# Kernel optimization log

Hardware: AMD Instinct MI355X
Metric: run time of the kernel (lower is better)

Reference implementation:

```python
import jax, jax.numpy as jnp
import numpy as np

T, B, N_LABELS = 128, 512, 512
HIDDEN, SEMANTIC = 1024, 1024
THRESHOLD, DECAY = 1.0, 0.95


def setup_inputs() -> dict:
    key = jax.random.key(0)
    k1, k2, k3 = jax.random.split(key, 3)
    spike_seq = (jax.random.uniform(k1, (T, B, N_LABELS)) < 0.1).astype(jnp.float32)
    W1 = jax.random.normal(k2, (HIDDEN, N_LABELS), dtype=jnp.float32) * 0.05
    W2 = jax.random.normal(k3, (SEMANTIC, HIDDEN), dtype=jnp.float32) * 0.05
    return {"spike_seq": spike_seq, "W1": W1, "W2": W2}


def reference(spike_seq, W1, W2):
    """LIF two-layer SNN. LIF step: v = decay*v + input; spike = (v > threshold);
    hard reset to zero on spike. Returns time-averaged spikes of layer1 and layer2."""
    dtype = spike_seq.dtype
    Bsz = spike_seq.shape[1]

    def lif(v, x):
        v = DECAY * v + x
        spk = (v > THRESHOLD).astype(dtype)
        return spk, v * (1.0 - spk)

    def step(carry, x_t):
        v1, v2 = carry
        spk1, v1 = lif(v1, x_t @ W1.T)          # (B, HIDDEN)
        spk2, v2 = lif(v2, spk1 @ W2.T)         # (B, SEMANTIC)
        return (v1, v2), (spk1, spk2)

    v1_0 = jnp.zeros((Bsz, W1.shape[0]), dtype)
    v2_0 = jnp.zeros((Bsz, W2.shape[0]), dtype)
    _, (spk1_all, spk2_all) = jax.lax.scan(step, (v1_0, v2_0), spike_seq)
    return spk1_all.mean(axis=0), spk2_all.mean(axis=0)
```

## Files before the change

kernel.cpp:

```cpp
#include <hip/hip_runtime.h>


#define T_STEPS 128
#define BATCH   512
#define NLAB    512
#define HID     1024
#define SEM     1024
#define KCW     5

__global__ __launch_bounds__(256) void transpose32(const float* __restrict__ in,
                                                   float* __restrict__ out,
                                                   int R, int C) {
    __shared__ float tile[32][33];
    const int c0 = blockIdx.x * 32, r0 = blockIdx.y * 32;
    const int x = threadIdx.x, y0 = threadIdx.y;
#pragma unroll
    for (int i = 0; i < 32; i += 8)
        tile[y0 + i][x] = in[(size_t)(r0 + y0 + i) * C + (c0 + x)];
    __syncthreads();
#pragma unroll
    for (int i = 0; i < 32; i += 8)
        out[(size_t)(c0 + y0 + i) * R + (r0 + x)] = tile[x][y0 + i];
}

__device__ __forceinline__ float gather_chain(const int* __restrict__ list,
                                              int lo, int hi,
                                              const float* __restrict__ base,
                                              int tid, float s) {
    int k = lo;
    for (; k + 8 <= hi; k += 8) {
        float w[8];
#pragma unroll
        for (int j = 0; j < 8; ++j) {
            const int row = __builtin_amdgcn_readfirstlane(list[k + j]);
            w[j] = base[((size_t)row << 10) + tid];
        }
#pragma unroll
        for (int j = 0; j < 8; ++j)
            s = __fadd_rn(s, w[j]);
    }
    for (; k < hi; ++k) {
        const int row = __builtin_amdgcn_readfirstlane(list[k]);
        s = __fadd_rn(s, base[((size_t)row << 10) + tid]);
    }
    return s;
}

__global__ __launch_bounds__(1024, 8)
void snn_kernel(const float* __restrict__ spikes,
                const float* __restrict__ w1t,
                const float* __restrict__ w2t,
                float* __restrict__ out) {
    __shared__ int wc1[8];
    __shared__ int wc2[16];
    __shared__ __align__(16) int list1[NLAB];
    __shared__ __align__(16) int list2[HID];

    const int b    = blockIdx.x;
    const int tid  = threadIdx.x;
    const int w    = tid >> 6;
    const int lane = tid & 63;

    float v1 = 0.0f, v2 = 0.0f;
    int c1 = 0, c2 = 0;
    const float* sp_b = spikes + (size_t)b * NLAB;

    for (int t = 0; t < T_STEPS; ++t) {
        bool act = false;
        int pre1 = 0;
        if (tid < NLAB) {
            act = (sp_b[(size_t)t * (BATCH * NLAB) + tid] != 0.0f);
            const unsigned long long m = __ballot(act);
            pre1 = __popcll(m & ((1ull << lane) - 1ull));
            if (lane == 0) wc1[w] = __popcll(m);
        }
        __syncthreads();

        if (act) {
            int base = 0;
            for (int i = 0; i < w; ++i) base += wc1[i];
            list1[base + pre1] = tid;
        }
        __syncthreads();

        bool spk;
        int pre2 = 0;
        {
            int nA = 0, n1 = 0;
            {
                int s = 0;
#pragma unroll
                for (int i = 0; i < 8; ++i) { s += wc1[i]; if (i == KCW - 1) nA = s; }
                n1 = s;
            }
            const float x1 = __fadd_rn(gather_chain(list1, 0,  nA, w1t, tid, 0.0f),
                                       gather_chain(list1, nA, n1, w1t, tid, 0.0f));

            v1 = __fadd_rn(__fmul_rn(0.95f, v1), x1);
            spk = (v1 > 1.0f);
            if (spk) { c1++; v1 = 0.0f; }

            const unsigned long long m = __ballot(spk);
            pre2 = __popcll(m & ((1ull << lane) - 1ull));
            if (lane == 0) wc2[w] = __popcll(m);
        }
        __syncthreads();

        if (spk) {
            int base = 0;
            for (int i = 0; i < w; ++i) base += wc2[i];
            list2[base + pre2] = tid;
        }
        __syncthreads();

        {
            int nA = 0, nB = 0, nC = 0, n2 = 0;
            {
                int s = 0;
#pragma unroll
                for (int i = 0; i < 16; ++i) {
                    s += wc2[i];
                    if (i == KCW - 1)     nA = s;
                    if (i == 2 * KCW - 1) nB = s;
                    if (i == 3 * KCW - 1) nC = s;
                }
                n2 = s;
            }
            const float t1 = gather_chain(list2, 0,  nA, w2t, tid, 0.0f);
            const float t2 = gather_chain(list2, nA, nB, w2t, tid, 0.0f);
            const float t3 = gather_chain(list2, nB, nC, w2t, tid, 0.0f);
            const float t4 = gather_chain(list2, nC, n2, w2t, tid, 0.0f);
            const float x2 = __fadd_rn(__fadd_rn(__fadd_rn(t1, t2), t3), t4);

            v2 = __fadd_rn(__fmul_rn(0.95f, v2), x2);
            if (v2 > 1.0f) { c2++; v2 = 0.0f; }
        }
        __syncthreads();
    }

    out[(size_t)b * HID + tid]                       = (float)c1 * (1.0f / 128.0f);
    out[(size_t)BATCH * HID + (size_t)b * SEM + tid] = (float)c2 * (1.0f / 128.0f);
}

extern "C" void kernel_launch(void* const* d_in, const int* in_sizes, int n_in,
                              void* d_out, int out_size, void* d_ws, size_t ws_size,
                              hipStream_t stream) {
    const float* spikes = (const float*)d_in[0];
    const float* W1     = (const float*)d_in[1];
    const float* W2     = (const float*)d_in[2];
    float* out = (float*)d_out;

    float* w1t = (float*)d_ws;
    float* w2t = w1t + (size_t)NLAB * HID;

    dim3 tb(32, 8);
    transpose32<<<dim3(NLAB / 32, HID / 32), tb, 0, stream>>>(W1, w1t, HID, NLAB);
    transpose32<<<dim3(HID / 32, SEM / 32),  tb, 0, stream>>>(W2, w2t, SEM, HID);

    snn_kernel<<<BATCH, 1024, 0, stream>>>(spikes, w1t, w2t, out);
}
```

Baseline: 1.767 ms.

## Use 256-thread blocks with four neurons per thread and float4 weight gathers

Shrinks each block from 1024 to 256 threads, with every thread now owning four consecutive hidden or semantic neurons. Weight rows are gathered as float4 and spike inputs are read as float2. The compaction lists, ballots and chain split points are rebuilt so the summation order matches the earlier split. The aim is fewer, wider memory transactions and cheaper barriers across fewer waves, at the cost of more registers per thread and less latency hiding from wave count.

```diff
diff --git a/kernel.cpp b/kernel.cpp
--- a/kernel.cpp
+++ b/kernel.cpp
@@ -6,7 +6,6 @@
 #define NLAB    512
 #define HID     1024
 #define SEM     1024
-#define KCW     5
 
 __global__ __launch_bounds__(256) void transpose32(const float* __restrict__ in,
                                                    float* __restrict__ out,
@@ -23,36 +22,47 @@
         out[(size_t)(c0 + y0 + i) * R + (r0 + x)] = tile[x][y0 + i];
 }
 
-__device__ __forceinline__ float gather_chain(const int* __restrict__ list,
-                                              int lo, int hi,
-                                              const float* __restrict__ base,
-                                              int tid, float s) {
+__device__ __forceinline__ void gather4(const int* __restrict__ list,
+                                        int lo, int hi,
+                                        const float* __restrict__ base,
+                                        float s[4]) {
+    float s0 = 0.0f, s1 = 0.0f, s2 = 0.0f, s3 = 0.0f;
     int k = lo;
     for (; k + 8 <= hi; k += 8) {
-        float w[8];
+        float4 wv[8];
 #pragma unroll
         for (int j = 0; j < 8; ++j) {
             const int row = __builtin_amdgcn_readfirstlane(list[k + j]);
-            w[j] = base[((size_t)row << 10) + tid];
-        }
-#pragma unroll
-        for (int j = 0; j < 8; ++j)
-            s = __fadd_rn(s, w[j]);
+            wv[j] = *reinterpret_cast<const float4*>(base + ((size_t)row << 10));
+        }
+#pragma unroll
+        for (int j = 0; j < 8; ++j) {
+            s0 = __fadd_rn(s0, wv[j].x);
+            s1 = __fadd_rn(s1, wv[j].y);
+            s2 = __fadd_rn(s2, wv[j].z);
+            s3 = __fadd_rn(s3, wv[j].w);
+        }
     }
     for (; k < hi; ++k) {
         const int row = __builtin_amdgcn_readfirstlane(list[k]);
-        s = __fadd_rn(s, base[((size_t)row << 10) + tid]);
+        const float4 wv = *reinterpret_cast<const float4*>(base + ((size_t)row << 10));
+        s0 = __fadd_rn(s0, wv.x);
+        s1 = __fadd_rn(s1, wv.y);
+        s2 = __fadd_rn(s2, wv.z);
+        s3 = __fadd_rn(s3, wv.w);
     }
-    return s;
-}
-
-__global__ __launch_bounds__(1024, 8)
+    s[0] = s0; s[1] = s1; s[2] = s2; s[3] = s3;
+}
+
+__global__ __launch_bounds__(256)
 void snn_kernel(const float* __restrict__ spikes,
                 const float* __restrict__ w1t,
                 const float* __restrict__ w2t,
                 float* __restrict__ out) {
-    __shared__ int wc1[8];
-    __shared__ int wc2[16];
+    __shared__ int wc1[4];
+    __shared__ int wc1p;
+    __shared__ int wc2[4];
+    __shared__ int wc2p[3];
     __shared__ __align__(16) int list1[NLAB];
     __shared__ __align__(16) int list2[HID];
 
@@ -60,86 +70,117 @@
     const int tid  = threadIdx.x;
     const int w    = tid >> 6;
     const int lane = tid & 63;
-
-    float v1 = 0.0f, v2 = 0.0f;
-    int c1 = 0, c2 = 0;
-    const float* sp_b = spikes + (size_t)b * NLAB;
+    const unsigned long long below = (1ull << lane) - 1ull;
+
+    float v1[4] = {0.0f, 0.0f, 0.0f, 0.0f};
+    float v2[4] = {0.0f, 0.0f, 0.0f, 0.0f};
+    int   c1[4] = {0, 0, 0, 0};
+    int   c2[4] = {0, 0, 0, 0};
+
+    const float* sp_b = spikes + (size_t)b * NLAB + 2 * tid;
+    const float* w1b  = w1t + 4 * tid;
+    const float* w2b  = w2t + 4 * tid;
 
     for (int t = 0; t < T_STEPS; ++t) {
-        bool act = false;
-        int pre1 = 0;
-        if (tid < NLAB) {
-            act = (sp_b[(size_t)t * (BATCH * NLAB) + tid] != 0.0f);
-            const unsigned long long m = __ballot(act);
-            pre1 = __popcll(m & ((1ull << lane) - 1ull));
-            if (lane == 0) wc1[w] = __popcll(m);
-        }
-        __syncthreads();
-
-        if (act) {
+        const float2 sv = *reinterpret_cast<const float2*>(sp_b + (size_t)t * (BATCH * NLAB));
+        const bool a0 = (sv.x != 0.0f);
+        const bool a1 = (sv.y != 0.0f);
+        const unsigned long long m0 = __ballot(a0);
+        const unsigned long long m1 = __ballot(a1);
+        if (lane == 0) {
+            wc1[w] = __popcll(m0) + __popcll(m1);
+            if (w == 2)
+                wc1p = __popcll(m0 & 0xFFFFFFFFull) + __popcll(m1 & 0xFFFFFFFFull);
+        }
+        const int pre1 = __popcll(m0 & below) + __popcll(m1 & below);
+        __syncthreads();
+
+        {
             int base = 0;
             for (int i = 0; i < w; ++i) base += wc1[i];
-            list1[base + pre1] = tid;
-        }
-        __syncthreads();
-
-        bool spk;
-        int pre2 = 0;
-        {
-            int nA = 0, n1 = 0;
-            {
-                int s = 0;
-#pragma unroll
-                for (int i = 0; i < 8; ++i) { s += wc1[i]; if (i == KCW - 1) nA = s; }
-                n1 = s;
+            int p = base + pre1;
+            if (a0) list1[p++] = 2 * tid;
+            if (a1) list1[p]   = 2 * tid + 1;
+        }
+        __syncthreads();
+
+        bool spk0, spk1, spk2, spk3;
+        int  preh;
+        {
+            const int nA = wc1[0] + wc1[1] + wc1p;
+            const int n1 = wc1[0] + wc1[1] + wc1[2] + wc1[3];
+            float xA[4], xB[4];
+            gather4(list1, 0,  nA, w1b, xA);
+            gather4(list1, nA, n1, w1b, xB);
+#pragma unroll
+            for (int j = 0; j < 4; ++j) {
+                const float x1 = __fadd_rn(xA[j], xB[j]);
+                v1[j] = __fadd_rn(__fmul_rn(0.95f, v1[j]), x1);
             }
-            const float x1 = __fadd_rn(gather_chain(list1, 0,  nA, w1t, tid, 0.0f),
-                                       gather_chain(list1, nA, n1, w1t, tid, 0.0f));
-
-            v1 = __fadd_rn(__fmul_rn(0.95f, v1), x1);
-            spk = (v1 > 1.0f);
-            if (spk) { c1++; v1 = 0.0f; }
-
-            const unsigned long long m = __ballot(spk);
-            pre2 = __popcll(m & ((1ull << lane) - 1ull));
-            if (lane == 0) wc2[w] = __popcll(m);
-        }
-        __syncthreads();
-
-        if (spk) {
+            spk0 = (v1[0] > 1.0f); if (spk0) { c1[0]++; v1[0] = 0.0f; }
+            spk1 = (v1[1] > 1.0f); if (spk1) { c1[1]++; v1[1] = 0.0f; }
+            spk2 = (v1[2] > 1.0f); if (spk2) { c1[2]++; v1[2] = 0.0f; }
+            spk3 = (v1[3] > 1.0f); if (spk3) { c1[3]++; v1[3] = 0.0f; }
+
+            const unsigned long long b0 = __ballot(spk0);
+            const unsigned long long b1 = __ballot(spk1);
+            const unsigned long long b2 = __ballot(spk2);
+            const unsigned long long b3 = __ballot(spk3);
+            if (lane == 0) {
+                wc2[w] = __popcll(b0) + __popcll(b1) + __popcll(b2) + __popcll(b3);
+                if (w == 1)
+                    wc2p[0] = __popcll(b0 & 0xFFFFull) + __popcll(b1 & 0xFFFFull)
+                            + __popcll(b2 & 0xFFFFull) + __popcll(b3 & 0xFFFFull);
+                if (w == 2)
+                    wc2p[1] = __popcll(b0 & 0xFFFFFFFFull) + __popcll(b1 & 0xFFFFFFFFull)
+                            + __popcll(b2 & 0xFFFFFFFFull) + __popcll(b3 & 0xFFFFFFFFull);
+                if (w == 3)
+                    wc2p[2] = __popcll(b0 & 0xFFFFFFFFFFFFull) + __popcll(b1 & 0xFFFFFFFFFFFFull)
+                            + __popcll(b2 & 0xFFFFFFFFFFFFull) + __popcll(b3 & 0xFFFFFFFFFFFFull);
+            }
+            preh = __popcll(b0 & below) + __popcll(b1 & below)
+                 + __popcll(b2 & below) + __popcll(b3 & below);
+        }
+        __syncthreads();
+
+        {
             int base = 0;
             for (int i = 0; i < w; ++i) base += wc2[i];
-            list2[base + pre2] = tid;
-        }
-        __syncthreads();
-
-        {
-            int nA = 0, nB = 0, nC = 0, n2 = 0;
-            {
-                int s = 0;
-#pragma unroll
-                for (int i = 0; i < 16; ++i) {
-                    s += wc2[i];
-                    if (i == KCW - 1)     nA = s;
-                    if (i == 2 * KCW - 1) nB = s;
-                    if (i == 3 * KCW - 1) nC = s;
-                }
-                n2 = s;
+            int p = base + preh;
+            if (spk0) list2[p++] = 4 * tid;
+            if (spk1) list2[p++] = 4 * tid + 1;
+            if (spk2) list2[p++] = 4 * tid + 2;
+            if (spk3) list2[p]   = 4 * tid + 3;
+        }
+        __syncthreads();
+
+        {
+            const int nA = wc2[0] + wc2p[0];
+            const int nB = wc2[0] + wc2[1] + wc2p[1];
+            const int nC = wc2[0] + wc2[1] + wc2[2] + wc2p[2];
+            const int n2 = wc2[0] + wc2[1] + wc2[2] + wc2[3];
+            float t1[4], t2[4], t3[4], t4[4];
+            gather4(list2, 0,  nA, w2b, t1);
+            gather4(list2, nA, nB, w2b, t2);
+            gather4(list2, nB, nC, w2b, t3);
+            gather4(list2, nC, n2, w2b, t4);
+#pragma unroll
+            for (int j = 0; j < 4; ++j) {
+                const float x2 = __fadd_rn(__fadd_rn(__fadd_rn(t1[j], t2[j]), t3[j]), t4[j]);
+                v2[j] = __fadd_rn(__fmul_rn(0.95f, v2[j]), x2);
+                if (v2[j] > 1.0f) { c2[j]++; v2[j] = 0.0f; }
             }
-            const float t1 = gather_chain(list2, 0,  nA, w2t, tid, 0.0f);
-            const float t2 = gather_chain(list2, nA, nB, w2t, tid, 0.0f);
-            const float t3 = gather_chain(list2, nB, nC, w2t, tid, 0.0f);
-            const float t4 = gather_chain(list2, nC, n2, w2t, tid, 0.0f);
-            const float x2 = __fadd_rn(__fadd_rn(__fadd_rn(t1, t2), t3), t4);
-
-            v2 = __fadd_rn(__fmul_rn(0.95f, v2), x2);
-            if (v2 > 1.0f) { c2++; v2 = 0.0f; }
         }
         __syncthreads();
     }
 
-    out[(size_t)b * HID + tid]                       = (float)c1 * (1.0f / 128.0f);
-    out[(size_t)BATCH * HID + (size_t)b * SEM + tid] = (float)c2 * (1.0f / 128.0f);
+    const float sc = 1.0f / 128.0f;
+    const float4 o1 = make_float4((float)c1[0] * sc, (float)c1[1] * sc,
+                                  (float)c1[2] * sc, (float)c1[3] * sc);
+    *reinterpret_cast<float4*>(out + (size_t)b * HID + 4 * tid) = o1;
+    const float4 o2 = make_float4((float)c2[0] * sc, (float)c2[1] * sc,
+                                  (float)c2[2] * sc, (float)c2[3] * sc);
+    *reinterpret_cast<float4*>(out + (size_t)BATCH * HID + (size_t)b * SEM + 4 * tid) = o2;
 }
 
 extern "C" void kernel_launch(void* const* d_in, const int* in_sizes, int n_in,
@@ -157,5 +198,5 @@
     transpose32<<<dim3(NLAB / 32, HID / 32), tb, 0, stream>>>(W1, w1t, HID, NLAB);
     transpose32<<<dim3(HID / 32, SEM / 32),  tb, 0, stream>>>(W2, w2t, SEM, HID);
 
-    snn_kernel<<<BATCH, 1024, 0, stream>>>(spikes, w1t, w2t, out);
-}
+    snn_kernel<<<BATCH, 256, 0, stream>>>(spikes, w1t, w2t, out);
+}
```

New measurement: 1.613 ms. 8.7% less time.

## Process two batch rows per block with union spike lists and float2 weight gathers

Applied to the files above, without the earlier changes.

Each block now handles two batch elements with 512 threads, and each thread owns two output neurons. The sparse input and hidden spike lists are built over the union of both rows, with per-row flag bits, so each gathered weight row is loaded once and serves both batch elements through masked FMAs. Weight loads become float2, and the next timestep's spike input is prefetched. The aim is to halve redundant weight-row traffic and list-building overhead. In exchange, list lengths grow to the union of both rows and each thread does more FMAs per step. Chain splits are kept aligned to mimic the original summation order.

```diff
diff --git a/kernel.cpp b/kernel.cpp
--- a/kernel.cpp
+++ b/kernel.cpp
@@ -6,7 +6,6 @@
 #define NLAB    512
 #define HID     1024
 #define SEM     1024
-#define KCW     5
 
 __global__ __launch_bounds__(256) void transpose32(const float* __restrict__ in,
                                                    float* __restrict__ out,
@@ -23,123 +22,199 @@
         out[(size_t)(c0 + y0 + i) * R + (r0 + x)] = tile[x][y0 + i];
 }
 
-__device__ __forceinline__ float gather_chain(const int* __restrict__ list,
-                                              int lo, int hi,
-                                              const float* __restrict__ base,
-                                              int tid, float s) {
+__device__ __forceinline__ void gather22(const int* __restrict__ list,
+                                         int lo, int hi,
+                                         const float* __restrict__ base,
+                                         float s[4]) {
+    float s0 = 0.0f, s1 = 0.0f, s2 = 0.0f, s3 = 0.0f;
     int k = lo;
+    for (; k + 16 <= hi; k += 16) {
+        float2 wv[16];
+        int    e[16];
+#pragma unroll
+        for (int j = 0; j < 16; ++j) {
+            e[j] = __builtin_amdgcn_readfirstlane(list[k + j]);
+            wv[j] = *reinterpret_cast<const float2*>(base + ((size_t)(e[j] & 0xFFFF) << 10));
+        }
+#pragma unroll
+        for (int j = 0; j < 16; ++j) {
+            const float f0 = (e[j] & 0x10000) ? 1.0f : 0.0f;
+            const float f1 = (e[j] & 0x20000) ? 1.0f : 0.0f;
+            s0 = __fmaf_rn(f0, wv[j].x, s0);
+            s1 = __fmaf_rn(f0, wv[j].y, s1);
+            s2 = __fmaf_rn(f1, wv[j].x, s2);
+            s3 = __fmaf_rn(f1, wv[j].y, s3);
+        }
+    }
     for (; k + 8 <= hi; k += 8) {
-        float w[8];
+        float2 wv[8];
+        int    e[8];
 #pragma unroll
         for (int j = 0; j < 8; ++j) {
-            const int row = __builtin_amdgcn_readfirstlane(list[k + j]);
-            w[j] = base[((size_t)row << 10) + tid];
-        }
-#pragma unroll
-        for (int j = 0; j < 8; ++j)
-            s = __fadd_rn(s, w[j]);
+            e[j] = __builtin_amdgcn_readfirstlane(list[k + j]);
+            wv[j] = *reinterpret_cast<const float2*>(base + ((size_t)(e[j] & 0xFFFF) << 10));
+        }
+#pragma unroll
+        for (int j = 0; j < 8; ++j) {
+            const float f0 = (e[j] & 0x10000) ? 1.0f : 0.0f;
+            const float f1 = (e[j] & 0x20000) ? 1.0f : 0.0f;
+            s0 = __fmaf_rn(f0, wv[j].x, s0);
+            s1 = __fmaf_rn(f0, wv[j].y, s1);
+            s2 = __fmaf_rn(f1, wv[j].x, s2);
+            s3 = __fmaf_rn(f1, wv[j].y, s3);
+        }
     }
     for (; k < hi; ++k) {
-        const int row = __builtin_amdgcn_readfirstlane(list[k]);
-        s = __fadd_rn(s, base[((size_t)row << 10) + tid]);
-    }
-    return s;
-}
-
-__global__ __launch_bounds__(1024, 8)
+        const int e = __builtin_amdgcn_readfirstlane(list[k]);
+        const float2 wv = *reinterpret_cast<const float2*>(base + ((size_t)(e & 0xFFFF) << 10));
+        const float f0 = (e & 0x10000) ? 1.0f : 0.0f;
+        const float f1 = (e & 0x20000) ? 1.0f : 0.0f;
+        s0 = __fmaf_rn(f0, wv.x, s0);
+        s1 = __fmaf_rn(f0, wv.y, s1);
+        s2 = __fmaf_rn(f1, wv.x, s2);
+        s3 = __fmaf_rn(f1, wv.y, s3);
+    }
+    s[0] = s0; s[1] = s1; s[2] = s2; s[3] = s3;
+}
+
+__global__ __launch_bounds__(512)
 void snn_kernel(const float* __restrict__ spikes,
                 const float* __restrict__ w1t,
                 const float* __restrict__ w2t,
                 float* __restrict__ out) {
     __shared__ int wc1[8];
-    __shared__ int wc2[16];
+    __shared__ int wc2[8];
+    __shared__ int wc2pA;
+    __shared__ int wc2pC;
     __shared__ __align__(16) int list1[NLAB];
     __shared__ __align__(16) int list2[HID];
 
-    const int b    = blockIdx.x;
     const int tid  = threadIdx.x;
     const int w    = tid >> 6;
     const int lane = tid & 63;
-
-    float v1 = 0.0f, v2 = 0.0f;
-    int c1 = 0, c2 = 0;
-    const float* sp_b = spikes + (size_t)b * NLAB;
+    const unsigned long long below = (1ull << lane) - 1ull;
+
+    const int b0 = 2 * blockIdx.x;
+
+    float v1[4] = {0.0f, 0.0f, 0.0f, 0.0f};
+    float v2[4] = {0.0f, 0.0f, 0.0f, 0.0f};
+    int   c1[4] = {0, 0, 0, 0};
+    int   c2[4] = {0, 0, 0, 0};
+
+    const float* sp0 = spikes + (size_t)b0 * NLAB + tid;
+    const float* sp1 = sp0 + NLAB;
+    const float* w1b = w1t + 2 * tid;
+    const float* w2b = w2t + 2 * tid;
+
+    float sv0 = *sp0;
+    float sv1 = *sp1;
 
     for (int t = 0; t < T_STEPS; ++t) {
-        bool act = false;
-        int pre1 = 0;
-        if (tid < NLAB) {
-            act = (sp_b[(size_t)t * (BATCH * NLAB) + tid] != 0.0f);
-            const unsigned long long m = __ballot(act);
-            pre1 = __popcll(m & ((1ull << lane) - 1ull));
-            if (lane == 0) wc1[w] = __popcll(m);
-        }
-        __syncthreads();
-
-        if (act) {
+        const bool a0 = (sv0 != 0.0f);
+        const bool a1 = (sv1 != 0.0f);
+        const bool u  = a0 | a1;
+        const unsigned long long mu = __ballot(u);
+        if (lane == 0) wc1[w] = __popcll(mu);
+        const int pre1 = __popcll(mu & below);
+        __syncthreads();
+
+        if (u) {
             int base = 0;
             for (int i = 0; i < w; ++i) base += wc1[i];
-            list1[base + pre1] = tid;
-        }
-        __syncthreads();
-
-        bool spk;
-        int pre2 = 0;
+            list1[base + pre1] = tid | (a0 ? 0x10000 : 0) | (a1 ? 0x20000 : 0);
+        }
+        __syncthreads();
+
+        if (t + 1 < T_STEPS) {
+            sv0 = sp0[(size_t)(t + 1) * (BATCH * NLAB)];
+            sv1 = sp1[(size_t)(t + 1) * (BATCH * NLAB)];
+        }
+
+        bool s00, s01, s10, s11;
+        int  preh;
         {
             int nA = 0, n1 = 0;
             {
                 int s = 0;
 #pragma unroll
-                for (int i = 0; i < 8; ++i) { s += wc1[i]; if (i == KCW - 1) nA = s; }
+                for (int i = 0; i < 8; ++i) { s += wc1[i]; if (i == 4) nA = s; }
                 n1 = s;
             }
-            const float x1 = __fadd_rn(gather_chain(list1, 0,  nA, w1t, tid, 0.0f),
-                                       gather_chain(list1, nA, n1, w1t, tid, 0.0f));
-
-            v1 = __fadd_rn(__fmul_rn(0.95f, v1), x1);
-            spk = (v1 > 1.0f);
-            if (spk) { c1++; v1 = 0.0f; }
-
-            const unsigned long long m = __ballot(spk);
-            pre2 = __popcll(m & ((1ull << lane) - 1ull));
-            if (lane == 0) wc2[w] = __popcll(m);
-        }
-        __syncthreads();
-
-        if (spk) {
+            float xA[4], xB[4];
+            gather22(list1, 0,  nA, w1b, xA);
+            gather22(list1, nA, n1, w1b, xB);
+#pragma unroll
+            for (int j = 0; j < 4; ++j) {
+                const float x1 = __fadd_rn(xA[j], xB[j]);
+                v1[j] = __fadd_rn(__fmul_rn(0.95f, v1[j]), x1);
+            }
+            s00 = (v1[0] > 1.0f); if (s00) { c1[0]++; v1[0] = 0.0f; }
+            s01 = (v1[1] > 1.0f); if (s01) { c1[1]++; v1[1] = 0.0f; }
+            s10 = (v1[2] > 1.0f); if (s10) { c1[2]++; v1[2] = 0.0f; }
+            s11 = (v1[3] > 1.0f); if (s11) { c1[3]++; v1[3] = 0.0f; }
+
+            const bool u0 = s00 | s10;
+            const bool u1 = s01 | s11;
+            const unsigned long long m0 = __ballot(u0);
+            const unsigned long long m1 = __ballot(u1);
+            if (lane == 0) {
+                wc2[w] = __popcll(m0) + __popcll(m1);
+                if (w == 2)
+                    wc2pA = __popcll(m0 & 0xFFFFFFFFull) + __popcll(m1 & 0xFFFFFFFFull);
+                if (w == 7)
+                    wc2pC = __popcll(m0 & 0xFFFFFFFFull) + __popcll(m1 & 0xFFFFFFFFull);
+            }
+            preh = __popcll(m0 & below) + __popcll(m1 & below);
+
+            __syncthreads();
+
             int base = 0;
             for (int i = 0; i < w; ++i) base += wc2[i];
-            list2[base + pre2] = tid;
+            int p = base + preh;
+            if (u0) list2[p++] = (2 * tid)     | (s00 ? 0x10000 : 0) | (s10 ? 0x20000 : 0);
+            if (u1) list2[p]   = (2 * tid + 1) | (s01 ? 0x10000 : 0) | (s11 ? 0x20000 : 0);
         }
         __syncthreads();
 
         {
-            int nA = 0, nB = 0, nC = 0, n2 = 0;
+            int nA, nB = 0, nC, n2 = 0;
             {
                 int s = 0;
 #pragma unroll
-                for (int i = 0; i < 16; ++i) {
-                    s += wc2[i];
-                    if (i == KCW - 1)     nA = s;
-                    if (i == 2 * KCW - 1) nB = s;
-                    if (i == 3 * KCW - 1) nC = s;
-                }
+                for (int i = 0; i < 8; ++i) { s += wc2[i]; if (i == 4) nB = s; }
                 n2 = s;
             }
-            const float t1 = gather_chain(list2, 0,  nA, w2t, tid, 0.0f);
-            const float t2 = gather_chain(list2, nA, nB, w2t, tid, 0.0f);
-            const float t3 = gather_chain(list2, nB, nC, w2t, tid, 0.0f);
-            const float t4 = gather_chain(list2, nC, n2, w2t, tid, 0.0f);
-            const float x2 = __fadd_rn(__fadd_rn(__fadd_rn(t1, t2), t3), t4);
-
-            v2 = __fadd_rn(__fmul_rn(0.95f, v2), x2);
-            if (v2 > 1.0f) { c2++; v2 = 0.0f; }
-        }
-        __syncthreads();
-    }
-
-    out[(size_t)b * HID + tid]                       = (float)c1 * (1.0f / 128.0f);
-    out[(size_t)BATCH * HID + (size_t)b * SEM + tid] = (float)c2 * (1.0f / 128.0f);
+            nA = wc2[0] + wc2[1] + wc2pA;
+            nC = wc2[0] + wc2[1] + wc2[2] + wc2[3] + wc2[4] + wc2[5] + wc2[6] + wc2pC;
+            float t1[4], t2[4], t3[4], t4[4];
+            gather22(list2, 0,  nA, w2b, t1);
+            gather22(list2, nA, nB, w2b, t2);
+            gather22(list2, nB, nC, w2b, t3);
+            gather22(list2, nC, n2, w2b, t4);
+#pragma unroll
+            for (int j = 0; j < 4; ++j) {
+                const float x2 = __fadd_rn(__fadd_rn(__fadd_rn(t1[j], t2[j]), t3[j]), t4[j]);
+                v2[j] = __fadd_rn(__fmul_rn(0.95f, v2[j]), x2);
+                if (v2[j] > 1.0f) { c2[j]++; v2[j] = 0.0f; }
+            }
+        }
+        __syncthreads();
+    }
+
+    const float sc = 1.0f / 128.0f;
+    {
+        const float2 o0 = make_float2((float)c1[0] * sc, (float)c1[1] * sc);
+        const float2 o1 = make_float2((float)c1[2] * sc, (float)c1[3] * sc);
+        *reinterpret_cast<float2*>(out + (size_t)b0 * HID + 2 * tid)       = o0;
+        *reinterpret_cast<float2*>(out + (size_t)(b0 + 1) * HID + 2 * tid) = o1;
+    }
+    {
+        float* o2b = out + (size_t)BATCH * HID;
+        const float2 o0 = make_float2((float)c2[0] * sc, (float)c2[1] * sc);
+        const float2 o1 = make_float2((float)c2[2] * sc, (float)c2[3] * sc);
+        *reinterpret_cast<float2*>(o2b + (size_t)b0 * SEM + 2 * tid)       = o0;
+        *reinterpret_cast<float2*>(o2b + (size_t)(b0 + 1) * SEM + 2 * tid) = o1;
+    }
 }
 
 extern "C" void kernel_launch(void* const* d_in, const int* in_sizes, int n_in,
@@ -157,5 +232,5 @@
     transpose32<<<dim3(NLAB / 32, HID / 32), tb, 0, stream>>>(W1, w1t, HID, NLAB);
     transpose32<<<dim3(HID / 32, SEM / 32),  tb, 0, stream>>>(W2, w2t, SEM, HID);
 
-    snn_kernel<<<BATCH, 1024, 0, stream>>>(spikes, w1t, w2t, out);
-}
+    snn_kernel<<<BATCH / 2, 512, 0, stream>>>(spikes, w1t, w2t, out);
+}
```

Measured after the change: 2.166 ms. 22.6% more time.
